# Kernel tuning notes

Measured on AMD Instinct MI355X. Metric: run time of the kernel, lower is better.

## Reference

```python
import jax, jax.numpy as jnp
import numpy as np

C = 512
NUM_HEADS = 8
HEAD_DIM = C // NUM_HEADS
GROUPS = 32
EPS = 1e-5


def setup_inputs() -> dict:
    key = jax.random.key(0)
    ks = jax.random.split(key, 7)
    N, H, W = 16, 32, 32
    x = jax.random.normal(ks[0], (N, C, H, W), dtype=jnp.float32)
    norm_w = jax.random.normal(ks[1], (C,), dtype=jnp.float32) * 0.02 + 1.0
    norm_b = jax.random.normal(ks[2], (C,), dtype=jnp.float32) * 0.02
    qkv_w = jax.random.normal(ks[3], (3 * C, C), dtype=jnp.float32) * (1.0 / np.sqrt(C))
    qkv_b = jax.random.normal(ks[4], (3 * C,), dtype=jnp.float32) * 0.02
    proj_w = jax.random.normal(ks[5], (C, C), dtype=jnp.float32) * (1.0 / np.sqrt(C))
    proj_b = jax.random.normal(ks[6], (C,), dtype=jnp.float32) * 0.02
    return {"x": x, "norm_w": norm_w, "norm_b": norm_b, "qkv_w": qkv_w,
            "qkv_b": qkv_b, "proj_w": proj_w, "proj_b": proj_b}


def _group_norm(x, w, b):
    N, Cc, H, W = x.shape
    xg = x.reshape(N, GROUPS, Cc // GROUPS, H, W)
    mean = xg.mean(axis=(2, 3, 4), keepdims=True)
    var = xg.var(axis=(2, 3, 4), keepdims=True)
    xg = (xg - mean) * jax.lax.rsqrt(var + EPS)
    return xg.reshape(N, Cc, H, W) * w[None, :, None, None] + b[None, :, None, None]


def reference(x, norm_w, norm_b, qkv_w, qkv_b, proj_w, proj_b):
    N, Cc, H, W = x.shape
    S = H * W
    h = _group_norm(x, norm_w, norm_b)
    # 1x1 conv == per-pixel linear over channels
    qkv = jnp.einsum('nchw,oc->nohw', h, qkv_w) + qkv_b[None, :, None, None]
    q, k, v = jnp.split(qkv, 3, axis=1)  # each [N, C, H, W]
    # [N, heads, head_dim, S]
    q = q.reshape(N, NUM_HEADS, HEAD_DIM, S)
    k = k.reshape(N, NUM_HEADS, HEAD_DIM, S)
    v = v.reshape(N, NUM_HEADS, HEAD_DIM, S)
    scale = HEAD_DIM ** -0.5
    attn = jnp.einsum('nhds,nhdt->nhst', q, k) * scale  # [N,heads,S,S]
    attn = jax.nn.softmax(attn, axis=-1)
    out = jnp.einsum('nhst,nhdt->nhds', attn, v)  # [N,heads,head_dim,S]
    out = out.reshape(N, Cc, H, W)
    out = jnp.einsum('nchw,oc->nohw', out, proj_w) + proj_b[None, :, None, None]
    return out + x
```

## Files before the change

kernel.cpp:

```cpp
#include <hip/hip_runtime.h>
#include <cstdint>
#include <cstddef>

typedef unsigned short u16;
typedef __attribute__((ext_vector_type(8))) short bf16x8;
typedef __attribute__((ext_vector_type(4))) short bf16x4;
typedef __attribute__((ext_vector_type(4))) float f32x4;
typedef __attribute__((ext_vector_type(16))) float f32x16;
typedef __attribute__((ext_vector_type(4))) unsigned short u16x4;

#define NB 16
#define CD 512
#define SD 1024
#define NH 8
#define HD 64

#define QSCL 0.18033688011112042f

__device__ __forceinline__ u16 f2bf(float f) {
    unsigned u = __float_as_uint(f);
    u += 0x7FFF + ((u >> 16) & 1);
    return (u16)(u >> 16);
}
__device__ __forceinline__ unsigned cvt_pk(float lo, float hi) {
    unsigned r;
    asm("v_cvt_pk_bf16_f32 %0, %1, %2" : "=v"(r) : "v"(lo), "v"(hi));
    return r;
}
__device__ __forceinline__ float exp2v(float x) {
    float r;
    asm("v_exp_f32 %0, %1" : "=v"(r) : "v"(x));
    return r;
}
__device__ __forceinline__ void gload16(const void* g, void* l) {
    __builtin_amdgcn_global_load_lds(
        (const __attribute__((address_space(1))) void*)g,
        (__attribute__((address_space(3))) void*)l, 16, 0, 0);
}

__global__ __launch_bounds__(256) void cvt2_kernel(
    const float* __restrict__ s0, u16* __restrict__ d0,
    const float* __restrict__ s1, u16* __restrict__ d1)
{
    const int bid = blockIdx.x;
    const float* s;
    u16* d;
    int i;
    if (bid < 768) { s = s0; d = d0; i = (bid * 256 + threadIdx.x) * 4; }
    else           { s = s1; d = d1; i = ((bid - 768) * 256 + threadIdx.x) * 4; }
    float4 v = *reinterpret_cast<const float4*>(s + i);
    u16x4 o = { f2bf(v.x), f2bf(v.y), f2bf(v.z), f2bf(v.w) };
    *reinterpret_cast<u16x4*>(d + i) = o;
}

__global__ __launch_bounds__(256) void gn_kernel(
    const float* __restrict__ x, const float* __restrict__ w,
    const float* __restrict__ b, u16* __restrict__ h)
{
    const int n = blockIdx.x >> 5, g = blockIdx.x & 31;
    const size_t base = ((size_t)n * CD + g * 16) * SD;
    const float4* xp = reinterpret_cast<const float4*>(x + base);

    float4 vals[16];
    float sum = 0.f, ss = 0.f;
#pragma unroll
    for (int i = 0; i < 16; ++i) {
        float4 v = xp[threadIdx.x + (i << 8)];
        vals[i] = v;
        sum += v.x + v.y + v.z + v.w;
        ss  += v.x*v.x + v.y*v.y + v.z*v.z + v.w*v.w;
    }
#pragma unroll
    for (int off = 32; off > 0; off >>= 1) {
        sum += __shfl_down(sum, off);
        ss  += __shfl_down(ss,  off);
    }
    __shared__ float rs[4], rq[4];
    const int wid = threadIdx.x >> 6, lane = threadIdx.x & 63;
    if (lane == 0) { rs[wid] = sum; rq[wid] = ss; }
    __syncthreads();
    const float tsum = rs[0] + rs[1] + rs[2] + rs[3];
    const float tss  = rq[0] + rq[1] + rq[2] + rq[3];
    const float mean = tsum * (1.0f / 16384.0f);
    const float var  = tss * (1.0f / 16384.0f) - mean * mean;
    const float inv  = rsqrtf(var + 1e-5f);

    u16* hp = h + ((size_t)n * SD + 4 * threadIdx.x) * CD + g * 16;
#pragma unroll
    for (int i = 0; i < 16; ++i) {
        const float A  = inv * w[g * 16 + i];
        const float Bc = b[g * 16 + i] - mean * A;
        float4 v = vals[i];
        hp[i]          = f2bf(v.x * A + Bc);
        hp[CD + i]     = f2bf(v.y * A + Bc);
        hp[2 * CD + i] = f2bf(v.z * A + Bc);
        hp[3 * CD + i] = f2bf(v.w * A + Bc);
    }
}

template<int MODE>
__global__ __launch_bounds__(256) void mfma_gemm(
    const u16* __restrict__ Wb, const u16* __restrict__ act,
    const float* __restrict__ bias, const float* __restrict__ resid,
    void* __restrict__ outp, u16* __restrict__ vtout, int M)
{
    const int nb = blockIdx.z, m0 = blockIdx.y * 128, s0 = blockIdx.x * 128;
    __shared__ u16 Al[128 * 64];
    __shared__ u16 Bl[128 * 64];
    const int tid = threadIdx.x, wv = tid >> 6, ln = tid & 63;
    const int wm = wv >> 1, wn = wv & 1, lr = ln & 15, lg = ln >> 4;

    const f32x4 zero = {0.f, 0.f, 0.f, 0.f};
    f32x4 acc[4][4];
#pragma unroll
    for (int i = 0; i < 4; ++i)
#pragma unroll
        for (int j = 0; j < 4; ++j) acc[i][j] = zero;

    const u16* Ab = Wb + (size_t)m0 * CD;
    const u16* Bb = act + ((size_t)nb * SD + s0) * CD;

    for (int k0 = 0; k0 < CD; k0 += 64) {
        __syncthreads();
#pragma unroll
        for (int r = 0; r < 4; ++r) {
            const int gi = (r * 4 + wv) * 64 + ln;
            const int row = gi >> 3, gc = gi & 7;
            const int sg = ((gc ^ (row & 7)) * 8);
            gload16(Ab + (size_t)row * CD + k0 + sg, Al + gi * 8);
            gload16(Bb + (size_t)row * CD + k0 + sg, Bl + gi * 8);
        }
        __syncthreads();

#pragma unroll
        for (int kc = 0; kc < 2; ++kc) {
            bf16x8 af[4], bfr[4];
#pragma unroll
            for (int mi = 0; mi < 4; ++mi) {
                const int row = wm * 64 + mi * 16 + lr;
                af[mi] = *reinterpret_cast<const bf16x8*>(
                    Al + row * 64 + (((kc * 4 + lg) ^ (row & 7)) * 8));
            }
#pragma unroll
            for (int nj = 0; nj < 4; ++nj) {
                const int row = wn * 64 + nj * 16 + lr;
                bfr[nj] = *reinterpret_cast<const bf16x8*>(
                    Bl + row * 64 + (((kc * 4 + lg) ^ (row & 7)) * 8));
            }
#pragma unroll
            for (int mi = 0; mi < 4; ++mi)
#pragma unroll
                for (int nj = 0; nj < 4; ++nj) {
                    if (MODE == 0)
                        acc[mi][nj] = __builtin_amdgcn_mfma_f32_16x16x32_bf16(
                            af[mi], bfr[nj], acc[mi][nj], 0, 0, 0);
                    else
                        acc[mi][nj] = __builtin_amdgcn_mfma_f32_16x16x32_bf16(
                            bfr[mi], af[nj], acc[mi][nj], 0, 0, 0);
                }
        }
    }

    if (MODE == 0) {
        if (m0 < 1024) {
            u16* o = (u16*)outp;
            const float sc = (m0 < 512) ? QSCL : 1.0f;
#pragma unroll
            for (int mi = 0; mi < 4; ++mi) {
                const int mb = m0 + wm * 64 + mi * 16 + lg * 4;
#pragma unroll
                for (int nj = 0; nj < 4; ++nj) {
                    const int s = s0 + wn * 64 + nj * 16 + lr;
                    u16x4 pack;
#pragma unroll
                    for (int r = 0; r < 4; ++r)
                        pack[r] = f2bf((acc[mi][nj][r] + bias[mb + r]) * sc);
                    *reinterpret_cast<u16x4*>(o + ((size_t)nb * SD + s) * 1024 + mb) = pack;
                }
            }
        } else {
            const int sswap = (lg >= 2) ? 4 : 0;
#pragma unroll
            for (int mi = 0; mi < 4; ++mi)
#pragma unroll
                for (int r = 0; r < 4; ++r) {
                    const int m = m0 + wm * 64 + mi * 16 + lg * 4 + r;
                    const float bi = bias[m];
#pragma unroll
                    for (int nj = 0; nj < 4; ++nj) {
                        const int s = (s0 + wn * 64 + nj * 16 + lr) ^ sswap;
                        vtout[((size_t)nb * 512 + (m - 1024)) * SD + s] = f2bf(acc[mi][nj][r] + bi);
                    }
                }
        }
    } else {
        float* o = (float*)outp;
#pragma unroll
        for (int i = 0; i < 4; ++i)
#pragma unroll
            for (int j = 0; j < 4; ++j) {
                const int m = m0 + wm * 64 + j * 16 + lr;
                const int s = s0 + wn * 64 + i * 16 + lg * 4;
                const float bi = bias[m];
                const size_t idx = ((size_t)nb * M + m) * SD + s;
                float4 r4 = *reinterpret_cast<const float4*>(resid + idx);
                float4 v;
                v.x = acc[i][j][0] + bi + r4.x;
                v.y = acc[i][j][1] + bi + r4.y;
                v.z = acc[i][j][2] + bi + r4.z;
                v.w = acc[i][j][3] + bi + r4.w;
                *reinterpret_cast<float4*>(o + idx) = v;
            }
    }
}

__global__ __launch_bounds__(256) void attn_mfma(
    const u16* __restrict__ qk, const u16* __restrict__ vt, u16* __restrict__ ao)
{
    const int nh = blockIdx.x, n = nh >> 3, hh = nh & 7;
    const int q0 = blockIdx.y << 7;
    const int tid = threadIdx.x, wv = tid >> 6, ln = tid & 63;
    const int lq = ln & 31, hi = ln >> 5;

    __shared__ u16 Kl[2][64 * 64];
    __shared__ u16 Vl[2][64 * 64];

    const u16* Qb = qk + (size_t)n * SD * 1024 + hh * HD;
    const u16* Kb = Qb + 512;
    const u16* Vb = vt + ((size_t)n * 512 + hh * HD) * SD;

    bf16x8 qf[4];
    {
        const u16* qp = Qb + (size_t)(q0 + wv * 32 + lq) * 1024 + hi * 8;
#pragma unroll
        for (int ks = 0; ks < 4; ++ks)
            qf[ks] = *reinterpret_cast<const bf16x8*>(qp + ks * 16);
    }

    f32x16 of0 = {}, of1 = {};
    float mrun = -INFINITY, lrun = 0.f;

    const int i0 = tid, i1 = tid + 256;
    const int sr0 = i0 >> 3, g0 = ((i0 & 7) ^ (sr0 & 7)) * 8;
    const int sr1 = i1 >> 3, g1 = ((i1 & 7) ^ (sr1 & 7)) * 8;
    const u16* Ks0 = Kb + (size_t)sr0 * 1024 + g0;
    const u16* Ks1 = Kb + (size_t)sr1 * 1024 + g1;
    const u16* Vs0 = Vb + (size_t)sr0 * SD + g0;
    const u16* Vs1 = Vb + (size_t)sr1 * SD + g1;

    gload16(Ks0, &Kl[0][i0 * 8]);  gload16(Ks1, &Kl[0][i1 * 8]);
    gload16(Vs0, &Vl[0][i0 * 8]);  gload16(Vs1, &Vl[0][i1 * 8]);
    __syncthreads();

    const int hkey = (hi ^ ((lq >> 3) & 1)) * 4;
    int cur = 0;
    for (int tt = 0; tt < 16; ++tt) {
        if (tt < 15) {
            const int t1 = (tt + 1) << 6;
            gload16(Ks0 + (size_t)t1 * 1024, &Kl[cur ^ 1][i0 * 8]);
            gload16(Ks1 + (size_t)t1 * 1024, &Kl[cur ^ 1][i1 * 8]);
            gload16(Vs0 + t1, &Vl[cur ^ 1][i0 * 8]);
            gload16(Vs1 + t1, &Vl[cur ^ 1][i1 * 8]);
        }
        f32x16 st0 = {}, st1 = {};
        const u16* Kc = &Kl[cur][0];
        __builtin_amdgcn_s_setprio(1);
#pragma unroll
        for (int ks = 0; ks < 4; ++ks) {
            const int g = (((ks * 2 + hi) ^ (lq & 7)) * 8);
            bf16x8 k0 = *reinterpret_cast<const bf16x8*>(Kc + lq * 64 + g);
            bf16x8 k1 = *reinterpret_cast<const bf16x8*>(Kc + (32 + lq) * 64 + g);
            st0 = __builtin_amdgcn_mfma_f32_32x32x16_bf16(k0, qf[ks], st0, 0, 0, 0);
            st1 = __builtin_amdgcn_mfma_f32_32x32x16_bf16(k1, qf[ks], st1, 0, 0, 0);
        }
        __builtin_amdgcn_s_setprio(0);
        float tm[8];
#pragma unroll
        for (int i = 0; i < 8; ++i)
            tm[i] = fmaxf(fmaxf(st0[i], st0[i + 8]), fmaxf(st1[i], st1[i + 8]));
        float mx = fmaxf(fmaxf(fmaxf(tm[0], tm[1]), fmaxf(tm[2], tm[3])),
                         fmaxf(fmaxf(tm[4], tm[5]), fmaxf(tm[6], tm[7])));
        mx = fmaxf(mx, __shfl_xor(mx, 32));
        if (!__all(mx - mrun <= 8.0f)) {
            const float mn = fmaxf(mrun, mx);
            const float al = exp2v(mrun - mn);
            mrun = mn;
            lrun *= al;
#pragma unroll
            for (int r = 0; r < 16; ++r) { of0[r] *= al; of1[r] *= al; }
        }
        float sa = 0.f, sb = 0.f, sc = 0.f, sd = 0.f;
#pragma unroll
        for (int r = 0; r < 16; r += 4) {
            st0[r]     = exp2v(st0[r]     - mrun); sa += st0[r];
            st0[r + 1] = exp2v(st0[r + 1] - mrun); sb += st0[r + 1];
            st0[r + 2] = exp2v(st0[r + 2] - mrun); sc += st0[r + 2];
            st0[r + 3] = exp2v(st0[r + 3] - mrun); sd += st0[r + 3];
        }
#pragma unroll
        for (int r = 0; r < 16; r += 4) {
            st1[r]     = exp2v(st1[r]     - mrun); sa += st1[r];
            st1[r + 1] = exp2v(st1[r + 1] - mrun); sb += st1[r + 1];
            st1[r + 2] = exp2v(st1[r + 2] - mrun); sc += st1[r + 2];
            st1[r + 3] = exp2v(st1[r + 3] - mrun); sd += st1[r + 3];
        }
        float ps = (sa + sb) + (sc + sd);
        ps += __shfl_xor(ps, 32);
        lrun += ps;

        const u16* Vc = &Vl[cur][0];
        __builtin_amdgcn_s_setprio(1);
#pragma unroll
        for (int ks = 0; ks < 4; ++ks) {
            union { unsigned w[4]; bf16x8 v; } pf;
            const int rb = (ks & 1) * 8;
            if (ks < 2) {
                pf.w[0] = cvt_pk(st0[rb + 0], st0[rb + 1]);
                pf.w[1] = cvt_pk(st0[rb + 2], st0[rb + 3]);
                pf.w[2] = cvt_pk(st0[rb + 4], st0[rb + 5]);
                pf.w[3] = cvt_pk(st0[rb + 6], st0[rb + 7]);
            } else {
                pf.w[0] = cvt_pk(st1[rb + 0], st1[rb + 1]);
                pf.w[1] = cvt_pk(st1[rb + 2], st1[rb + 3]);
                pf.w[2] = cvt_pk(st1[rb + 4], st1[rb + 5]);
                pf.w[3] = cvt_pk(st1[rb + 6], st1[rb + 7]);
            }
            const int e0 = ((2 * ks) ^ (lq & 7)) * 8 + hkey;
            const int e1 = ((2 * ks + 1) ^ (lq & 7)) * 8 + hkey;
            union { bf16x4 h[2]; bf16x8 v; } vf0, vf1;
            vf0.h[0] = *reinterpret_cast<const bf16x4*>(Vc + lq * 64 + e0);
            vf0.h[1] = *reinterpret_cast<const bf16x4*>(Vc + lq * 64 + e1);
            vf1.h[0] = *reinterpret_cast<const bf16x4*>(Vc + (32 + lq) * 64 + e0);
            vf1.h[1] = *reinterpret_cast<const bf16x4*>(Vc + (32 + lq) * 64 + e1);
            of0 = __builtin_amdgcn_mfma_f32_32x32x16_bf16(vf0.v, pf.v, of0, 0, 0, 0);
            of1 = __builtin_amdgcn_mfma_f32_32x32x16_bf16(vf1.v, pf.v, of1, 0, 0, 0);
        }
        __builtin_amdgcn_s_setprio(0);
        __syncthreads();
        cur ^= 1;
    }

    const float inv = 1.0f / lrun;
    u16* op = ao + ((size_t)n * SD + q0 + wv * 32 + lq) * CD + hh * HD;
#pragma unroll
    for (int g = 0; g < 4; ++g) {
        u16x4 o0, o1;
#pragma unroll
        for (int e = 0; e < 4; ++e) {
            o0[e] = f2bf(of0[g * 4 + e] * inv);
            o1[e] = f2bf(of1[g * 4 + e] * inv);
        }
        const int d0 = g * 8 + hi * 4;
        *reinterpret_cast<u16x4*>(op + d0) = o0;
        *reinterpret_cast<u16x4*>(op + 32 + d0) = o1;
    }
}

extern "C" void kernel_launch(void* const* d_in, const int* in_sizes, int n_in,
                              void* d_out, int out_size, void* d_ws, size_t ws_size,
                              hipStream_t stream)
{
    const float* x      = (const float*)d_in[0];
    const float* norm_w = (const float*)d_in[1];
    const float* norm_b = (const float*)d_in[2];
    const float* qkv_w  = (const float*)d_in[3];
    const float* qkv_b  = (const float*)d_in[4];
    const float* proj_w = (const float*)d_in[5];
    const float* proj_b = (const float*)d_in[6];

    u16* h   = (u16*)d_ws;
    u16* qkb = h + (size_t)NB * SD * CD;
    u16* vtb = qkb + (size_t)NB * SD * 1024;
    u16* ao  = vtb + (size_t)NB * 512 * SD;
    u16* wq  = ao + (size_t)NB * SD * CD;
    u16* wp  = wq + (size_t)1536 * CD;

    hipLaunchKernelGGL(cvt2_kernel, dim3(1024), dim3(256), 0, stream,
                       qkv_w, wq, proj_w, wp);
    hipLaunchKernelGGL(gn_kernel, dim3(NB * 32), dim3(256), 0, stream, x, norm_w, norm_b, h);
    hipLaunchKernelGGL((mfma_gemm<0>), dim3(8, 12, NB), dim3(256), 0, stream,
                       wq, h, qkv_b, (const float*)nullptr, (void*)qkb, vtb, 1536);
    hipLaunchKernelGGL(attn_mfma, dim3(NB * NH, SD / 128), dim3(256), 0, stream,
                       qkb, vtb, ao);
    hipLaunchKernelGGL((mfma_gemm<1>), dim3(8, 4, NB), dim3(256), 0, stream,
                       wp, ao, proj_b, x, (void*)d_out, (u16*)nullptr, 512);
}
```

Before: 248.6 us.

## Enlarge attention blocks to 256 queries, hint GEMM occupancy, simplify V store indexing

The attention kernel now runs 512 threads per block and covers 256 queries, so each K/V tile staged in shared memory is reused by eight waves instead of four. Each thread issues one K and one V async load per tile instead of two. The grid order is swapped so query blocks of the same head are adjacent. The GEMM gets a min-blocks-per-CU launch bound of 4, and the V-transpose store hoists its address and bias arithmetic. The risks are fewer attention blocks and waves per CU, plus register pressure from the occupancy hint.

```diff
diff --git a/kernel.cpp b/kernel.cpp
--- a/kernel.cpp
+++ b/kernel.cpp
@@ -99,7 +99,7 @@
 }
 
 template<int MODE>
-__global__ __launch_bounds__(256) void mfma_gemm(
+__global__ __launch_bounds__(256, 4) void mfma_gemm(
     const u16* __restrict__ Wb, const u16* __restrict__ act,
     const float* __restrict__ bias, const float* __restrict__ resid,
     void* __restrict__ outp, u16* __restrict__ vtout, int M)
@@ -180,17 +180,19 @@
             }
         } else {
             const int sswap = (lg >= 2) ? 4 : 0;
+            const int sbase = (s0 + wn * 64 + lr) ^ sswap;
+            const int mb = m0 - 1024 + wm * 64 + lg * 4;
+            u16* vb = vtout + ((size_t)nb * 512 + mb) * SD + sbase;
+            const float* bp = bias + m0 + wm * 64 + lg * 4;
 #pragma unroll
             for (int mi = 0; mi < 4; ++mi)
 #pragma unroll
                 for (int r = 0; r < 4; ++r) {
-                    const int m = m0 + wm * 64 + mi * 16 + lg * 4 + r;
-                    const float bi = bias[m];
-#pragma unroll
-                    for (int nj = 0; nj < 4; ++nj) {
-                        const int s = (s0 + wn * 64 + nj * 16 + lr) ^ sswap;
-                        vtout[((size_t)nb * 512 + (m - 1024)) * SD + s] = f2bf(acc[mi][nj][r] + bi);
-                    }
+                    const float bi = bp[mi * 16 + r];
+#pragma unroll
+                    for (int nj = 0; nj < 4; ++nj)
+                        vb[(size_t)(mi * 16 + r) * SD + nj * 16] =
+                            f2bf(acc[mi][nj][r] + bi);
                 }
         }
     } else {
@@ -214,11 +216,11 @@
     }
 }
 
-__global__ __launch_bounds__(256) void attn_mfma(
+__global__ __launch_bounds__(512) void attn_mfma(
     const u16* __restrict__ qk, const u16* __restrict__ vt, u16* __restrict__ ao)
 {
-    const int nh = blockIdx.x, n = nh >> 3, hh = nh & 7;
-    const int q0 = blockIdx.y << 7;
+    const int nh = blockIdx.y, n = nh >> 3, hh = nh & 7;
+    const int q0 = blockIdx.x << 8;
     const int tid = threadIdx.x, wv = tid >> 6, ln = tid & 63;
     const int lq = ln & 31, hi = ln >> 5;
 
@@ -240,16 +242,13 @@
     f32x16 of0 = {}, of1 = {};
     float mrun = -INFINITY, lrun = 0.f;
 
-    const int i0 = tid, i1 = tid + 256;
-    const int sr0 = i0 >> 3, g0 = ((i0 & 7) ^ (sr0 & 7)) * 8;
-    const int sr1 = i1 >> 3, g1 = ((i1 & 7) ^ (sr1 & 7)) * 8;
-    const u16* Ks0 = Kb + (size_t)sr0 * 1024 + g0;
-    const u16* Ks1 = Kb + (size_t)sr1 * 1024 + g1;
-    const u16* Vs0 = Vb + (size_t)sr0 * SD + g0;
-    const u16* Vs1 = Vb + (size_t)sr1 * SD + g1;
-
-    gload16(Ks0, &Kl[0][i0 * 8]);  gload16(Ks1, &Kl[0][i1 * 8]);
-    gload16(Vs0, &Vl[0][i0 * 8]);  gload16(Vs1, &Vl[0][i1 * 8]);
+    const int srow = tid >> 3, sgc = tid & 7;
+    const int ssw = (sgc ^ (srow & 7)) * 8;
+    const u16* Ksrc = Kb + (size_t)srow * 1024 + ssw;
+    const u16* Vsrc = Vb + (size_t)srow * SD + ssw;
+
+    gload16(Ksrc, &Kl[0][tid * 8]);
+    gload16(Vsrc, &Vl[0][tid * 8]);
     __syncthreads();
 
     const int hkey = (hi ^ ((lq >> 3) & 1)) * 4;
@@ -257,10 +256,8 @@
     for (int tt = 0; tt < 16; ++tt) {
         if (tt < 15) {
             const int t1 = (tt + 1) << 6;
-            gload16(Ks0 + (size_t)t1 * 1024, &Kl[cur ^ 1][i0 * 8]);
-            gload16(Ks1 + (size_t)t1 * 1024, &Kl[cur ^ 1][i1 * 8]);
-            gload16(Vs0 + t1, &Vl[cur ^ 1][i0 * 8]);
-            gload16(Vs1 + t1, &Vl[cur ^ 1][i1 * 8]);
+            gload16(Ksrc + (size_t)t1 * 1024, &Kl[cur ^ 1][tid * 8]);
+            gload16(Vsrc + t1, &Vl[cur ^ 1][tid * 8]);
         }
         f32x16 st0 = {}, st1 = {};
         const u16* Kc = &Kl[cur][0];
@@ -380,7 +377,7 @@
     hipLaunchKernelGGL(gn_kernel, dim3(NB * 32), dim3(256), 0, stream, x, norm_w, norm_b, h);
     hipLaunchKernelGGL((mfma_gemm<0>), dim3(8, 12, NB), dim3(256), 0, stream,
                        wq, h, qkv_b, (const float*)nullptr, (void*)qkb, vtb, 1536);
-    hipLaunchKernelGGL(attn_mfma, dim3(NB * NH, SD / 128), dim3(256), 0, stream,
+    hipLaunchKernelGGL(attn_mfma, dim3(SD / 256, NB * NH), dim3(512), 0, stream,
                        qkb, vtb, ao);
     hipLaunchKernelGGL((mfma_gemm<1>), dim3(8, 4, NB), dim3(256), 0, stream,
                        wp, ao, proj_b, x, (void*)d_out, (u16*)nullptr, 512);
```

After: 217.7 us. 12.4% less time.
